# Optimization experiments

Measured on AMD Instinct MI355X. Metric: run time of the kernel, lower is better.

## Reference

```python
import jax, jax.numpy as jnp
import numpy as np


def setup_inputs() -> dict:
    key = jax.random.key(0)
    ks = jax.random.split(key, 7)
    C = 512
    x = jax.random.normal(ks[0], (16, C, 64, 64), dtype=jnp.float32)
    wq = jax.random.normal(ks[1], (C, C), dtype=jnp.float32) * (1.0 / np.sqrt(C))
    bq = jax.random.normal(ks[2], (C,), dtype=jnp.float32) * 0.02
    wk = jax.random.normal(ks[3], (C, C), dtype=jnp.float32) * (1.0 / np.sqrt(C))
    bk = jax.random.normal(ks[4], (C,), dtype=jnp.float32) * 0.02
    wo = jax.random.normal(ks[5], (C, C), dtype=jnp.float32) * (1.0 / np.sqrt(C))
    bo = jax.random.normal(ks[6], (C,), dtype=jnp.float32) * 0.02
    return {"x": x, "wq": wq, "bq": bq, "wk": wk, "bk": bk, "wo": wo, "bo": bo, "num_heads": 8}


def _conv1x1(x, w, b):
    # 1x1 conv == per-pixel linear map over channels; w: [Cout, Cin]
    return jnp.einsum('oc,bchw->bohw', w, x) + b[None, :, None, None]


def reference(x, wq, bq, wk, bk, wo, bo, num_heads):
    B, C, H, W = x.shape
    dh = C // num_heads
    P = H * W  # spatial positions (tokens)
    q = _conv1x1(x, wq, bq).reshape(B, num_heads, dh, P)
    k = _conv1x1(x, wk, bk).reshape(B, num_heads, dh, P)
    v = x.reshape(B, num_heads, dh, P)
    # NOTE: faithful to the torch code, attention is [B, nh, dh, dh]
    # (channel-channel scores contracted over spatial positions).
    att = jnp.einsum('bndp,bnep->bnde', q, k) / jnp.sqrt(jnp.asarray(dh, x.dtype))
    att = jax.nn.softmax(att, axis=-1)
    out = jnp.einsum('bnde,bnep->bndp', att, v).reshape(B, C, H, W)
    out = _conv1x1(out, wo, bo)
    return out + x
```

## Files before the change

kernel.cpp:

```cpp
#include <hip/hip_runtime.h>


typedef unsigned short ushort_t;
typedef __attribute__((ext_vector_type(8))) short bf16x8;
typedef __attribute__((ext_vector_type(4))) float f32x4;
typedef __attribute__((ext_vector_type(4))) unsigned short us4;
typedef __attribute__((ext_vector_type(8))) unsigned short us8;

#define NB 16
#define NC 512
#define NP 4096
#define NHD 8
#define DH 64

#define BM 128
#define BN 128
#define BKK 64

__device__ inline ushort_t f2bf(float f) {
  unsigned int u = __float_as_uint(f);
  u += 0x7FFFu + ((u >> 16) & 1u);
  return (ushort_t)(u >> 16);
}
__device__ inline float bf2f(ushort_t h) {
  return __uint_as_float(((unsigned int)h) << 16);
}

__device__ inline void gld_lds16(const void* g, void* l) {
  __builtin_amdgcn_global_load_lds(
      (const __attribute__((address_space(1))) unsigned int*)g,
      (__attribute__((address_space(3))) unsigned int*)l, 16, 0, 0);
}

__global__ __launch_bounds__(256, 4) void k_mfma_bt(
    const ushort_t* __restrict__ A, const ushort_t* __restrict__ B,
    void* __restrict__ Cv, const float* __restrict__ bias,
    int lda, int ldb, int ldc, long long sA, long long sB, long long sC,
    int Kper, int mode, int flags) {
  __shared__ __align__(128) ushort_t Smem[16640];
  ushort_t* As = Smem;
  ushort_t* Bs = Smem + 8320;
  int m0, n0;
  long long zc;
  const ushort_t *Ab, *Bb;
  if (flags & 2) {
    int flat = blockIdx.x + 10 * blockIdx.z;
    int nf = (flat & 7) * 80 + (flat >> 3);
    int z2 = nf / 10, tile = nf - z2 * 10;
    int bb = z2 >> 2, sp = z2 & 3;
    int tm = (0x1A449000u >> (tile * 3)) & 7;
    int tn = (0x1B4D1688u >> (tile * 3)) & 7;
    m0 = tm * BM; n0 = tn * BN;
    Ab = A + bb * sA + (long long)sp * Kper;
    Bb = B + bb * sB + (long long)sp * Kper;
    zc = (long long)z2 * sC;
  } else {
    int bx = blockIdx.x, by = blockIdx.y;
    if (flags & 1) {
      int nxy = gridDim.x * gridDim.y;
      int id = bx + gridDim.x * by;
      int nid = (id & 7) * (nxy >> 3) + (id >> 3);
      bx = nid % gridDim.x; by = nid / gridDim.x;
    }
    m0 = by * BM; n0 = bx * BN;
    Ab = A + blockIdx.z * sA;
    Bb = B + blockIdx.z * sB;
    zc = (long long)blockIdx.z * sC;
  }
  int t = threadIdx.x;
  int lane = t & 63, w = t >> 6;
  int wr = w >> 1, wc = w & 1;
  int l15 = lane & 15, l4 = lane >> 4;
  int sr = lane >> 3, scc = lane & 7;

  f32x4 zero = {0.f, 0.f, 0.f, 0.f};
  f32x4 acc[4][4];
#pragma unroll
  for (int i = 0; i < 4; ++i)
#pragma unroll
    for (int j = 0; j < 4; ++j) acc[i][j] = zero;

  for (int k0 = 0; k0 < Kper; k0 += BKK) {
#pragma unroll
    for (int i = 0; i < 4; ++i) {
      int slab = w * 4 + i;
      int r = slab * 8 + sr;
      int kc = scc ^ (r & 7);
      gld_lds16(Ab + (size_t)(m0 + r) * lda + k0 + kc * 8, &As[slab * 512]);
      gld_lds16(Bb + (size_t)(n0 + r) * ldb + k0 + kc * 8, &Bs[slab * 512]);
    }
    __syncthreads();
#pragma unroll
    for (int kf = 0; kf < 2; ++kf) {
      bf16x8 av[4], bv[4];
#pragma unroll
      for (int i = 0; i < 4; ++i) {
        int r = wr * 64 + i * 16 + l15;
        int c = (kf * 4 + l4) ^ (r & 7);
        av[i] = *(const bf16x8*)&As[r * 64 + c * 8];
        int rn = wc * 64 + i * 16 + l15;
        int cn = (kf * 4 + l4) ^ (rn & 7);
        bv[i] = *(const bf16x8*)&Bs[rn * 64 + cn * 8];
      }
#pragma unroll
      for (int i = 0; i < 4; ++i)
#pragma unroll
        for (int j = 0; j < 4; ++j)
          acc[i][j] = __builtin_amdgcn_mfma_f32_16x16x32_bf16(av[i], bv[j],
                                                              acc[i][j], 0, 0, 0);
    }
    __syncthreads();
  }

  if (mode == 3) {
    ushort_t* C = (ushort_t*)Cv + zc;
#pragma unroll
    for (int i = 0; i < 4; ++i)
#pragma unroll
      for (int j = 0; j < 4; ++j)
#pragma unroll
        for (int rr = 0; rr < 4; ++rr) {
          int grow = m0 + wr * 64 + i * 16 + l4 * 4 + rr;
          int gcol = n0 + wc * 64 + j * 16 + l15;
          float v = acc[i][j][rr];
          ushort_t hi = f2bf(v);
          C[(size_t)grow * ldc + gcol] = hi;
          C[4194304 + (size_t)grow * ldc + gcol] = f2bf(v - bf2f(hi));
        }
  } else {
    float* C = (float*)Cv + zc;
    float* fbuf = (float*)Smem;
#pragma unroll
    for (int ch = 0; ch < 2; ++ch) {
      if (wr == ch) {
#pragma unroll
        for (int i = 0; i < 4; ++i)
#pragma unroll
          for (int j = 0; j < 4; ++j)
#pragma unroll
            for (int rr = 0; rr < 4; ++rr)
              fbuf[(i * 16 + l4 * 4 + rr) * 130 + wc * 64 + j * 16 + l15] =
                  acc[i][j][rr];
      }
      __syncthreads();
      {
        int row = t >> 2, q = t & 3;
        int grow = m0 + ch * 64 + row;
        float bb = (mode == 1) ? bias[grow] : 0.f;
        float* crow = C + (size_t)grow * ldc + n0 + q * 32;
#pragma unroll
        for (int u = 0; u < 8; ++u) {
          f32x4 v = *reinterpret_cast<const f32x4*>(&fbuf[row * 130 + q * 32 + u * 4]);
          v[0] += bb; v[1] += bb; v[2] += bb; v[3] += bb;
          if (mode == 1)
            __builtin_nontemporal_store(v, reinterpret_cast<f32x4*>(crow + u * 4));
          else
            *reinterpret_cast<f32x4*>(crow + u * 4) = v;
        }
      }
      __syncthreads();
    }
  }
}

__global__ __launch_bounds__(256) void k_prep(const float* __restrict__ x,
                                              ushort_t* __restrict__ xbf,
                                              ushort_t* __restrict__ xt,
                                              float* __restrict__ sPart) {
  __shared__ ushort_t ldsC[128 * 132];
  int b = blockIdx.z;
  int pp0 = blockIdx.x * 128, cc0 = blockIdx.y * 128;
  const float* xb = x + ((size_t)b * NC + cc0) * NP + pp0;
  int t = threadIdx.x;
  int rq = t >> 5;
  int q  = t & 31;
#pragma unroll
  for (int i = 0; i < 16; ++i) {
    int r = i * 8 + rq;
    float4 v = *reinterpret_cast<const float4*>(xb + (size_t)r * NP + q * 4);
    us4 u = {f2bf(v.x), f2bf(v.y), f2bf(v.z), f2bf(v.w)};
    *reinterpret_cast<us4*>(&xbf[((size_t)b * NC + cc0 + r) * NP + pp0 + q * 4]) = u;
    *reinterpret_cast<us4*>(&ldsC[r * 132 + q * 4]) = u;
    float s4 = (v.x + v.y) + (v.z + v.w);
    s4 += __shfl_xor(s4, 1, 32);
    s4 += __shfl_xor(s4, 2, 32);
    s4 += __shfl_xor(s4, 4, 32);
    s4 += __shfl_xor(s4, 8, 32);
    s4 += __shfl_xor(s4, 16, 32);
    if (q == 0) sPart[(size_t)blockIdx.x * (NB * NC) + b * NC + cc0 + r] = s4;
  }
  __syncthreads();
  int p = t >> 1, chalf = (t & 1) * 64;
  ushort_t* dst = &xt[((size_t)b * NP + pp0 + p) * NC + cc0 + chalf];
#pragma unroll
  for (int g = 0; g < 8; ++g) {
    us8 o;
#pragma unroll
    for (int j = 0; j < 8; ++j) o[j] = ldsC[(chalf + g * 8 + j) * 132 + p];
    *reinterpret_cast<us8*>(dst + g * 8) = o;
  }
}

__global__ __launch_bounds__(256) void k_sreduce(const float* __restrict__ sPart,
                                                 float* __restrict__ s) {
  int idx = blockIdx.x * 256 + threadIdx.x;
  float a = 0.f;
  for (int pb = 0; pb < 32; ++pb) a += sPart[(size_t)pb * (NB * NC) + idx];
  s[idx] = a;
}

__global__ __launch_bounds__(256) void k_cvtw(
    const float* __restrict__ wq, const float* __restrict__ wk,
    const float* __restrict__ wo, ushort_t* __restrict__ q,
    ushort_t* __restrict__ k, ushort_t* __restrict__ o) {
  int i = blockIdx.x * 256 + threadIdx.x;
  q[i] = f2bf(wq[i]);
  k[i] = f2bf(wk[i]);
  o[i] = f2bf(wo[i]);
}

__global__ __launch_bounds__(256) void k_reduceG(const float* __restrict__ Gp,
                                                 ushort_t* __restrict__ Gb) {
  __shared__ ushort_t ldsM[128 * 36];
  int slab = blockIdx.x, tile = blockIdx.y, b = blockIdx.z;
  int tm = (0x1A449000u >> (tile * 3)) & 7;
  int tn = (0x1B4D1688u >> (tile * 3)) & 7;
  int t = threadIdx.x;
  const float* base = Gp + ((size_t)b * 4) * 262144 +
                      (size_t)(tm * 128) * 512 + tn * 128 + slab * 32;
  ushort_t* gb = Gb + (size_t)b * 262144;
#pragma unroll
  for (int i = 0; i < 4; ++i) {
    int idx = i * 256 + t;
    int r = idx >> 3, lq = idx & 7;
    const float* p = base + (size_t)r * 512 + lq * 4;
    float4 v0 = *reinterpret_cast<const float4*>(p);
    float4 v1 = *reinterpret_cast<const float4*>(p + 262144);
    float4 v2 = *reinterpret_cast<const float4*>(p + 2 * 262144);
    float4 v3 = *reinterpret_cast<const float4*>(p + 3 * 262144);
    us4 u = {f2bf((v0.x + v1.x) + (v2.x + v3.x)),
             f2bf((v0.y + v1.y) + (v2.y + v3.y)),
             f2bf((v0.z + v1.z) + (v2.z + v3.z)),
             f2bf((v0.w + v1.w) + (v2.w + v3.w))};
    *reinterpret_cast<us4*>(
        &gb[(size_t)(tm * 128 + r) * 512 + tn * 128 + slab * 32 + lq * 4]) = u;
    if (tm != tn) *reinterpret_cast<us4*>(&ldsM[r * 36 + lq * 4]) = u;
  }
  if (tm == tn) return;
  __syncthreads();
  int orow = t >> 3, og = t & 7;
  ushort_t* dst = &gb[(size_t)(tn * 128 + slab * 32 + orow) * 512 + tm * 128 + og * 16];
#pragma unroll
  for (int h = 0; h < 2; ++h) {
    us8 o;
#pragma unroll
    for (int j = 0; j < 8; ++j) o[j] = ldsM[(og * 16 + h * 8 + j) * 36 + orow];
    *reinterpret_cast<us8*>(dst + h * 8) = o;
  }
}

__global__ __launch_bounds__(256) void k_uw(
    const float* __restrict__ wq, const float* __restrict__ wk,
    const float* __restrict__ s, float* __restrict__ U, float* __restrict__ W) {
  int b = blockIdx.x >> 3, n = blockIdx.x & 7;
  int t = threadIdx.x;
  __shared__ float ssh[NC];
  for (int i = t; i < NC; i += 256) ssh[i] = s[b * NC + i];
  __syncthreads();
  int pair = t >> 1, half = t & 1;
  int d = pair & 63, sel = pair >> 6;
  const float* row = (sel ? wk : wq) + (size_t)(n * DH + d) * NC + half * 256;
  const float* sb = ssh + half * 256;
  float a = 0.f;
#pragma unroll 8
  for (int i = 0; i < 64; ++i) {
    float4 v = reinterpret_cast<const float4*>(row)[i];
    a += v.x * sb[i * 4] + v.y * sb[i * 4 + 1] + v.z * sb[i * 4 + 2] +
         v.w * sb[i * 4 + 3];
  }
  a += __shfl_xor(a, 1, 64);
  if (half == 0) (sel ? W : U)[b * NC + n * DH + d] = a;
}

__global__ __launch_bounds__(256) void k_fused(
    const ushort_t* __restrict__ Thi, const ushort_t* __restrict__ Tlo,
    const ushort_t* __restrict__ Wkb, const ushort_t* __restrict__ Wob,
    const float* __restrict__ U, const float* __restrict__ Wv,
    const float* __restrict__ bq, const float* __restrict__ bk,
    ushort_t* __restrict__ Mb) {
  __shared__ __align__(128) ushort_t Th[64 * 64];
  __shared__ __align__(128) ushort_t Tl[64 * 64];
  __shared__ __align__(128) ushort_t Wks[64 * 64];
  __shared__ float Ps[64][65];
  __shared__ __align__(16) ushort_t PT[64 * 72];
  __shared__ __align__(128) ushort_t Wos[128 * 64];
  __shared__ float ush[64], wsh[64], bqs[64], bks[64];

  int b = blockIdx.x >> 4, n = (blockIdx.x >> 1) & 7, half = blockIdx.x & 1;
  int t = threadIdx.x, lane = t & 63, w = t >> 6;
  int l15 = lane & 15, l4 = lane >> 4;

  if (t < 64) ush[t] = U[b * NC + n * DH + t];
  else if (t < 128) wsh[t - 64] = Wv[b * NC + n * DH + (t - 64)];
  else if (t < 192) bqs[t - 128] = bq[n * DH + (t - 128)];
  else bks[t - 192] = bk[n * DH + (t - 192)];

  const size_t tbase = ((size_t)b * NC + n * DH) * NC;
  f32x4 zero = {0.f, 0.f, 0.f, 0.f};
  f32x4 acc[4];
#pragma unroll
  for (int i = 0; i < 4; ++i) acc[i] = zero;

  for (int kc0 = 0; kc0 < NC; kc0 += 64) {
    __syncthreads();
#pragma unroll
    for (int i = 0; i < 6; ++i) {
      int slab = w * 6 + i;
      int mat = slab >> 3, sl = slab & 7;
      int r = sl * 8 + (lane >> 3);
      int kc = (lane & 7) ^ (r & 7);
      if (mat == 0)
        gld_lds16(Thi + tbase + (size_t)r * NC + kc0 + kc * 8, &Th[sl * 512]);
      else if (mat == 1)
        gld_lds16(Tlo + tbase + (size_t)r * NC + kc0 + kc * 8, &Tl[sl * 512]);
      else
        gld_lds16(Wkb + (size_t)(n * DH + r) * NC + kc0 + kc * 8, &Wks[sl * 512]);
    }
    __syncthreads();
#pragma unroll
    for (int kf = 0; kf < 2; ++kf) {
      int rn = w * 16 + l15;
      int cn = (kf * 4 + l4) ^ (rn & 7);
      bf16x8 bvf = *(const bf16x8*)&Wks[rn * 64 + cn * 8];
#pragma unroll
      for (int i = 0; i < 4; ++i) {
        int r = i * 16 + l15;
        int c = (kf * 4 + l4) ^ (r & 7);
        bf16x8 ah = *(const bf16x8*)&Th[r * 64 + c * 8];
        bf16x8 al = *(const bf16x8*)&Tl[r * 64 + c * 8];
        acc[i] = __builtin_amdgcn_mfma_f32_16x16x32_bf16(ah, bvf, acc[i], 0, 0, 0);
        acc[i] = __builtin_amdgcn_mfma_f32_16x16x32_bf16(al, bvf, acc[i], 0, 0, 0);
      }
    }
  }
#pragma unroll
  for (int i = 0; i < 4; ++i)
#pragma unroll
    for (int rr = 0; rr < 4; ++rr) {
      int d = i * 16 + l4 * 4 + rr, e = w * 16 + l15;
      float v = acc[i][rr] + ush[d] * bks[e] + bqs[d] * (wsh[e] + 4096.f * bks[e]);
      Ps[d][e] = v * 0.125f;
    }
  __syncthreads();
  {
    int d = w * 16 + l15;
    float mx = -1e30f;
#pragma unroll
    for (int i = 0; i < 16; ++i) mx = fmaxf(mx, Ps[d][l4 * 16 + i]);
    mx = fmaxf(mx, __shfl_xor(mx, 16, 64));
    mx = fmaxf(mx, __shfl_xor(mx, 32, 64));
    float pv[16];
    float sum = 0.f;
#pragma unroll
    for (int i = 0; i < 16; ++i) {
      pv[i] = __expf(Ps[d][l4 * 16 + i] - mx);
      sum += pv[i];
    }
    sum += __shfl_xor(sum, 16, 64);
    sum += __shfl_xor(sum, 32, 64);
    float inv = 1.f / sum;
#pragma unroll
    for (int i = 0; i < 16; ++i) PT[(l4 * 16 + i) * 72 + d] = f2bf(pv[i] * inv);
  }
  for (int mi = 0; mi < 2; ++mi) {
    int mt = half * 2 + mi;
    __syncthreads();
#pragma unroll
    for (int i = 0; i < 4; ++i) {
      int slab = w * 4 + i;
      int r = slab * 8 + (lane >> 3);
      int kc = (lane & 7) ^ (r & 7);
      gld_lds16(Wob + (size_t)(mt * 128 + r) * NC + n * DH + kc * 8,
                &Wos[slab * 512]);
    }
    __syncthreads();
    f32x4 acc2[2][4];
#pragma unroll
    for (int i2 = 0; i2 < 2; ++i2)
#pragma unroll
      for (int j = 0; j < 4; ++j) acc2[i2][j] = zero;
#pragma unroll
    for (int kf = 0; kf < 2; ++kf) {
      bf16x8 bv[4];
#pragma unroll
      for (int j = 0; j < 4; ++j) {
        int e = j * 16 + l15;
        bv[j] = *(const bf16x8*)&PT[e * 72 + (kf * 4 + l4) * 8];
      }
#pragma unroll
      for (int i2 = 0; i2 < 2; ++i2) {
        int r = w * 32 + i2 * 16 + l15;
        int c = (kf * 4 + l4) ^ (r & 7);
        bf16x8 av = *(const bf16x8*)&Wos[r * 64 + c * 8];
#pragma unroll
        for (int j = 0; j < 4; ++j)
          acc2[i2][j] =
              __builtin_amdgcn_mfma_f32_16x16x32_bf16(av, bv[j], acc2[i2][j], 0, 0, 0);
      }
    }
#pragma unroll
    for (int i2 = 0; i2 < 2; ++i2)
#pragma unroll
      for (int j = 0; j < 4; ++j)
#pragma unroll
        for (int rr = 0; rr < 4; ++rr) {
          int grow = mt * 128 + w * 32 + i2 * 16 + l4 * 4 + rr;
          int gcol = n * DH + j * 16 + l15;
          float v = acc2[i2][j][rr];
          if (grow == gcol) v += 1.f;
          Mb[((size_t)b * NC + grow) * NC + gcol] = f2bf(v);
        }
  }
}

#define BKt 32
#define BMt 128
#define BNt 128
#define LDTK 132

__global__ __launch_bounds__(256) void k_rowsum(const float* __restrict__ x,
                                                float* __restrict__ s) {
  int row = blockIdx.x;
  const float* xr = x + (size_t)row * NP;
  int t = threadIdx.x;
  float acc = 0.f;
  for (int i = t; i < NP / 4; i += 256) {
    float4 v = reinterpret_cast<const float4*>(xr)[i];
    acc += (v.x + v.y) + (v.z + v.w);
  }
  for (int off = 32; off > 0; off >>= 1) acc += __shfl_down(acc, off, 64);
  __shared__ float red[4];
  int lane = t & 63, wv = t >> 6;
  if (lane == 0) red[wv] = acc;
  __syncthreads();
  if (t == 0) s[row] = (red[0] + red[1]) + (red[2] + red[3]);
}

__global__ __launch_bounds__(256) void k_gemm_abT(
    const float* __restrict__ Abase, const float* __restrict__ Bbase,
    float* __restrict__ Cbase, int K, int lda, int ldb, int ldc,
    size_t sA, size_t sB, size_t sC) {
  __shared__ float As[BKt][LDTK];
  __shared__ float Bs[BKt][LDTK];
  const float* A = Abase + sA * blockIdx.z;
  const float* Bm = Bbase + sB * blockIdx.z;
  float* Cm = Cbase + sC * blockIdx.z;
  int m0 = blockIdx.y * BMt, n0 = blockIdx.x * BNt;
  int t = threadIdx.x;
  int tr = t >> 4, tc = t & 15;
  float acc[8][8];
#pragma unroll
  for (int i = 0; i < 8; ++i)
#pragma unroll
    for (int j = 0; j < 8; ++j) acc[i][j] = 0.f;
  for (int k0 = 0; k0 < K; k0 += BKt) {
#pragma unroll
    for (int it = 0; it < 4; ++it) {
      int idx = it * 256 + t;
      int r = idx >> 3, kq = idx & 7;
      float4 va = *reinterpret_cast<const float4*>(A + (size_t)(m0 + r) * lda + k0 + kq * 4);
      As[kq * 4 + 0][r] = va.x; As[kq * 4 + 1][r] = va.y;
      As[kq * 4 + 2][r] = va.z; As[kq * 4 + 3][r] = va.w;
      float4 vb = *reinterpret_cast<const float4*>(Bm + (size_t)(n0 + r) * ldb + k0 + kq * 4);
      Bs[kq * 4 + 0][r] = vb.x; Bs[kq * 4 + 1][r] = vb.y;
      Bs[kq * 4 + 2][r] = vb.z; Bs[kq * 4 + 3][r] = vb.w;
    }
    __syncthreads();
#pragma unroll
    for (int kk = 0; kk < BKt; ++kk) {
      float4 a0 = *reinterpret_cast<const float4*>(&As[kk][tr * 8]);
      float4 a1 = *reinterpret_cast<const float4*>(&As[kk][tr * 8 + 4]);
      float4 b0 = *reinterpret_cast<const float4*>(&Bs[kk][tc * 8]);
      float4 b1 = *reinterpret_cast<const float4*>(&Bs[kk][tc * 8 + 4]);
      float av[8] = {a0.x, a0.y, a0.z, a0.w, a1.x, a1.y, a1.z, a1.w};
      float bv[8] = {b0.x, b0.y, b0.z, b0.w, b1.x, b1.y, b1.z, b1.w};
#pragma unroll
      for (int i = 0; i < 8; ++i)
#pragma unroll
        for (int j = 0; j < 8; ++j) acc[i][j] += av[i] * bv[j];
    }
    __syncthreads();
  }
#pragma unroll
  for (int i = 0; i < 8; ++i) {
    float* crow = Cm + (size_t)(m0 + tr * 8 + i) * ldc + n0 + tc * 8;
    float4 c0 = {acc[i][0], acc[i][1], acc[i][2], acc[i][3]};
    float4 c1 = {acc[i][4], acc[i][5], acc[i][6], acc[i][7]};
    *reinterpret_cast<float4*>(crow) = c0;
    *reinterpret_cast<float4*>(crow + 4) = c1;
  }
}

__global__ __launch_bounds__(256) void k_gemm_ab(
    const float* __restrict__ Abase, const float* __restrict__ Bbase,
    float* __restrict__ Cbase, const float* __restrict__ bias,
    int K, int lda, int ldb, int ldc, size_t sA, size_t sB, size_t sC) {
  __shared__ float As[BKt][LDTK];
  __shared__ float Bs[BKt][LDTK];
  const float* A = Abase + sA * blockIdx.z;
  const float* Bm = Bbase + sB * blockIdx.z;
  float* Cm = Cbase + sC * blockIdx.z;
  int m0 = blockIdx.y * BMt, n0 = blockIdx.x * BNt;
  int t = threadIdx.x;
  int tr = t >> 4, tc = t & 15;
  float acc[8][8];
#pragma unroll
  for (int i = 0; i < 8; ++i)
#pragma unroll
    for (int j = 0; j < 8; ++j) acc[i][j] = 0.f;
  for (int k0 = 0; k0 < K; k0 += BKt) {
#pragma unroll
    for (int it = 0; it < 4; ++it) {
      int idx = it * 256 + t;
      int r = idx >> 3, kq = idx & 7;
      float4 va = *reinterpret_cast<const float4*>(A + (size_t)(m0 + r) * lda + k0 + kq * 4);
      As[kq * 4 + 0][r] = va.x; As[kq * 4 + 1][r] = va.y;
      As[kq * 4 + 2][r] = va.z; As[kq * 4 + 3][r] = va.w;
      int kk = idx >> 5, nq = idx & 31;
      float4 vb = *reinterpret_cast<const float4*>(Bm + (size_t)(k0 + kk) * ldb + n0 + nq * 4);
      *reinterpret_cast<float4*>(&Bs[kk][nq * 4]) = vb;
    }
    __syncthreads();
#pragma unroll
    for (int kk = 0; kk < BKt; ++kk) {
      float4 a0 = *reinterpret_cast<const float4*>(&As[kk][tr * 8]);
      float4 a1 = *reinterpret_cast<const float4*>(&As[kk][tr * 8 + 4]);
      float4 b0 = *reinterpret_cast<const float4*>(&Bs[kk][tc * 8]);
      float4 b1 = *reinterpret_cast<const float4*>(&Bs[kk][tc * 8 + 4]);
      float av[8] = {a0.x, a0.y, a0.z, a0.w, a1.x, a1.y, a1.z, a1.w};
      float bv[8] = {b0.x, b0.y, b0.z, b0.w, b1.x, b1.y, b1.z, b1.w};
#pragma unroll
      for (int i = 0; i < 8; ++i)
#pragma unroll
        for (int j = 0; j < 8; ++j) acc[i][j] += av[i] * bv[j];
    }
    __syncthreads();
  }
#pragma unroll
  for (int i = 0; i < 8; ++i) {
    int row = m0 + tr * 8 + i;
    float bb = bias ? bias[row] : 0.f;
    float* crow = Cm + (size_t)row * ldc + n0 + tc * 8;
    float4 c0 = {acc[i][0] + bb, acc[i][1] + bb, acc[i][2] + bb, acc[i][3] + bb};
    float4 c1 = {acc[i][4] + bb, acc[i][5] + bb, acc[i][6] + bb, acc[i][7] + bb};
    *reinterpret_cast<float4*>(crow) = c0;
    *reinterpret_cast<float4*>(crow + 4) = c1;
  }
}

__global__ __launch_bounds__(256) void k_att(
    const float* __restrict__ T, const float* __restrict__ wq,
    const float* __restrict__ bq, const float* __restrict__ wk,
    const float* __restrict__ bk, const float* __restrict__ wo,
    const float* __restrict__ s, float* __restrict__ Mf) {
  int b = blockIdx.x >> 3, n = blockIdx.x & 7;
  int t = threadIdx.x;
  __shared__ float sh_s[NC];
  __shared__ float sh_u[DH], sh_w[DH];
  __shared__ float L[DH][DH + 1];
  __shared__ float Ts[DH][68];
  __shared__ float Ks[DH][68];

  for (int i = t; i < NC; i += 256) sh_s[i] = s[b * NC + i];
  __syncthreads();
  if (t < 128) {
    int d = t & 63;
    const float* wrow = (t < 64 ? wq : wk) + (size_t)(n * DH + d) * NC;
    float a = 0.f;
    for (int c = 0; c < NC; ++c) a += wrow[c] * sh_s[c];
    if (t < 64) sh_u[d] = a; else sh_w[d] = a;
  }

  int d = t >> 2, eg = t & 3;
  float acc[16];
#pragma unroll
  for (int i = 0; i < 16; ++i) acc[i] = 0.f;

  for (int c0 = 0; c0 < NC; c0 += 64) {
#pragma unroll
    for (int it = 0; it < 4; ++it) {
      int idx = it * 256 + t;
      int r = idx >> 4, cq = idx & 15;
      float4 v = *reinterpret_cast<const float4*>(
          T + ((size_t)b * NC + n * DH + r) * NC + c0 + cq * 4);
      *reinterpret_cast<float4*>(&Ts[r][cq * 4]) = v;
      float4 kv = *reinterpret_cast<const float4*>(
          wk + (size_t)(n * DH + r) * NC + c0 + cq * 4);
      Ks[cq * 4 + 0][r] = kv.x; Ks[cq * 4 + 1][r] = kv.y;
      Ks[cq * 4 + 2][r] = kv.z; Ks[cq * 4 + 3][r] = kv.w;
    }
    __syncthreads();
    for (int cc = 0; cc < 64; ++cc) {
      float tv = Ts[d][cc];
      float4 k0v = *reinterpret_cast<const float4*>(&Ks[cc][eg * 16]);
      float4 k1v = *reinterpret_cast<const float4*>(&Ks[cc][eg * 16 + 4]);
      float4 k2v = *reinterpret_cast<const float4*>(&Ks[cc][eg * 16 + 8]);
      float4 k3v = *reinterpret_cast<const float4*>(&Ks[cc][eg * 16 + 12]);
      acc[0] += tv * k0v.x;  acc[1] += tv * k0v.y;
      acc[2] += tv * k0v.z;  acc[3] += tv * k0v.w;
      acc[4] += tv * k1v.x;  acc[5] += tv * k1v.y;
      acc[6] += tv * k1v.z;  acc[7] += tv * k1v.w;
      acc[8] += tv * k2v.x;  acc[9] += tv * k2v.y;
      acc[10] += tv * k2v.z; acc[11] += tv * k2v.w;
      acc[12] += tv * k3v.x; acc[13] += tv * k3v.y;
      acc[14] += tv * k3v.z; acc[15] += tv * k3v.w;
    }
    __syncthreads();
  }

  float bqd = bq[n * DH + d];
  float ud = sh_u[d];
#pragma unroll
  for (int i = 0; i < 16; ++i) {
    int e = eg * 16 + i;
    float bke = bk[n * DH + e];
    L[d][e] = (acc[i] + ud * bke + bqd * (sh_w[e] + (float)NP * bke)) * 0.125f;
  }
  __syncthreads();
  if (t < 64) {
    float mx = -1e30f;
    for (int e = 0; e < DH; ++e) mx = fmaxf(mx, L[t][e]);
    float sum = 0.f;
    for (int e = 0; e < DH; ++e) { float p = __expf(L[t][e] - mx); L[t][e] = p; sum += p; }
    float inv = 1.f / sum;
    for (int e = 0; e < DH; ++e) L[t][e] *= inv;
  }
  __syncthreads();

#pragma unroll
  for (int rep = 0; rep < 2; ++rep) {
    int o = rep * 256 + t;
    const float* worow = wo + (size_t)o * NC + n * DH;
    float wreg[64];
#pragma unroll
    for (int q = 0; q < 16; ++q) {
      float4 v = *reinterpret_cast<const float4*>(worow + q * 4);
      wreg[q * 4 + 0] = v.x; wreg[q * 4 + 1] = v.y;
      wreg[q * 4 + 2] = v.z; wreg[q * 4 + 3] = v.w;
    }
    for (int e = 0; e < DH; ++e) {
      float a = 0.f;
#pragma unroll
      for (int dd = 0; dd < DH; ++dd) a += wreg[dd] * L[dd][e];
      int col = n * DH + e;
      if (o == col) a += 1.f;
      Mf[((size_t)b * NC + o) * NC + col] = a;
    }
  }
}

extern "C" void kernel_launch(void* const* d_in, const int* in_sizes, int n_in,
                              void* d_out, int out_size, void* d_ws, size_t ws_size,
                              hipStream_t stream) {
  const float* x  = (const float*)d_in[0];
  const float* wq = (const float*)d_in[1];
  const float* bq = (const float*)d_in[2];
  const float* wk = (const float*)d_in[3];
  const float* bk = (const float*)d_in[4];
  const float* wo = (const float*)d_in[5];
  const float* bo = (const float*)d_in[6];
  float* out = (float*)d_out;
  char* ws = (char*)d_ws;

  const size_t sX = (size_t)NC * NP;
  const size_t sG = (size_t)NC * NC;
  const size_t xbf_bytes = (size_t)NB * sX * 2;

  size_t off_s  = 0;
  size_t off_sp = 32768;
  size_t off_xt = off_sp + (size_t)64 * NB * NC * 4;
  size_t off_mb = off_xt + xbf_bytes;
  size_t off_wq = off_mb + (size_t)NB * sG * 2;
  size_t off_wk = off_wq + sG * 2;
  size_t off_wo = off_wk + sG * 2;
  size_t off_u  = off_wo + sG * 2;
  size_t off_w  = off_u + 32768;
  size_t need   = off_w + 32768;

  if (ws_size >= need + 4096) {
    float*    s     = (float*)(ws + off_s);
    float*    sPart = (float*)(ws + off_sp);
    ushort_t* Xt    = (ushort_t*)(ws + off_xt);
    ushort_t* Mb    = (ushort_t*)(ws + off_mb);
    ushort_t* Wqb   = (ushort_t*)(ws + off_wq);
    ushort_t* Wkb   = (ushort_t*)(ws + off_wk);
    ushort_t* Wob   = (ushort_t*)(ws + off_wo);
    float*    U     = (float*)(ws + off_u);
    float*    W     = (float*)(ws + off_w);
    char* dob = (char*)d_out;
    ushort_t* Xbf   = (ushort_t*)d_out;
    float*    Gpart = (float*)(dob + xbf_bytes);
    ushort_t* Gb    = (ushort_t*)d_out;
    ushort_t* Thi   = (ushort_t*)(dob + xbf_bytes);
    ushort_t* Tlo   = Thi + 4194304;

    k_cvtw<<<dim3(1024), 256, 0, stream>>>(wq, wk, wo, Wqb, Wkb, Wob);
    k_prep<<<dim3(32, 4, 16), 256, 0, stream>>>(x, Xbf, Xt, sPart);
    k_sreduce<<<dim3(32), 256, 0, stream>>>(sPart, s);
    k_uw<<<dim3(NB * NHD), 256, 0, stream>>>(wq, wk, s, U, W);
    k_mfma_bt<<<dim3(10, 1, 64), 256, 0, stream>>>(
        Xbf, Xbf, Gpart, nullptr, NP, NP, NC,
        (long long)sX, (long long)sX, (long long)sG, NP / 4, 2, 2);
    k_reduceG<<<dim3(4, 10, 16), 256, 0, stream>>>(Gpart, Gb);
    k_mfma_bt<<<dim3(4, 4, 16), 256, 0, stream>>>(
        Wqb, Gb, Thi, nullptr, NC, NC, NC,
        0LL, (long long)sG, (long long)sG, NC, 3, 1);
    k_fused<<<dim3(NB * NHD * 2), 256, 0, stream>>>(Thi, Tlo, Wkb, Wob, U, W,
                                                    bq, bk, Mb);
    k_mfma_bt<<<dim3(32, 4, 16), 256, 0, stream>>>(
        Mb, Xt, out, bo, NC, NC, NP,
        (long long)sG, (long long)sX, (long long)sX, NC, 1, 1);
  } else {
    float* s  = (float*)ws;
    float* G  = (float*)(ws + 32768);
    float* Tm = (float*)(ws + 32768 + (size_t)NB * sG * 4);
    float* M  = G;
    k_rowsum<<<NB * NC, 256, 0, stream>>>(x, s);
    k_gemm_abT<<<dim3(4, 4, NB), 256, 0, stream>>>(x, x, G, NP, NP, NP, NC, sX, sX, sG);
    k_gemm_ab<<<dim3(4, 4, NB), 256, 0, stream>>>(wq, G, Tm, nullptr, NC, NC, NC, NC,
                                                  0, sG, sG);
    k_att<<<NB * NHD, 256, 0, stream>>>(Tm, wq, bq, wk, bk, wo, s, M);
    k_gemm_ab<<<dim3(NP / BNt, NC / BMt, NB), 256, 0, stream>>>(M, x, out, bo, NC, NC,
                                                                NP, NP, sG, sX, sX);
  }
}
```

Measured before the change: 236.1 us.

## Split prep into row-wise convert+rowsum and separate bf16 transpose kernel

Replaces the fused convert/transpose/partial-sum prep kernel and its partial-sum reduction with two kernels. One converts each x row to bf16 and computes the full row sum directly. The other re-reads the bf16 tensor and transposes it through a larger LDS tile with nontemporal stores. This removes the partial-sum buffer and the extra reduction launch, but adds a second pass over the bf16 data (about 64MB read) in exchange for simpler, more coalesced access patterns.

```diff
diff --git a/kernel.cpp b/kernel.cpp
--- a/kernel.cpp
+++ b/kernel.cpp
@@ -163,50 +163,53 @@
   }
 }
 
-__global__ __launch_bounds__(256) void k_prep(const float* __restrict__ x,
-                                              ushort_t* __restrict__ xbf,
-                                              ushort_t* __restrict__ xt,
-                                              float* __restrict__ sPart) {
-  __shared__ ushort_t ldsC[128 * 132];
+__global__ __launch_bounds__(256) void k_cvt_rowsum(const float* __restrict__ x,
+                                                    ushort_t* __restrict__ xbf,
+                                                    float* __restrict__ s) {
+  int row = blockIdx.x;
+  const float* xr = x + (size_t)row * NP;
+  ushort_t* xo = xbf + (size_t)row * NP;
+  int t = threadIdx.x;
+  float acc = 0.f;
+#pragma unroll
+  for (int i = 0; i < 4; ++i) {
+    int idx = i * 256 + t;
+    float4 v = reinterpret_cast<const float4*>(xr)[idx];
+    us4 u = {f2bf(v.x), f2bf(v.y), f2bf(v.z), f2bf(v.w)};
+    reinterpret_cast<us4*>(xo)[idx] = u;
+    acc += (v.x + v.y) + (v.z + v.w);
+  }
+  for (int off = 32; off > 0; off >>= 1) acc += __shfl_down(acc, off, 64);
+  __shared__ float red[4];
+  if ((t & 63) == 0) red[t >> 6] = acc;
+  __syncthreads();
+  if (t == 0) s[row] = (red[0] + red[1]) + (red[2] + red[3]);
+}
+
+__global__ __launch_bounds__(256, 2) void k_transp(const ushort_t* __restrict__ xbf,
+                                                   ushort_t* __restrict__ xt) {
+  __shared__ ushort_t lds[256 * 128];
   int b = blockIdx.z;
-  int pp0 = blockIdx.x * 128, cc0 = blockIdx.y * 128;
-  const float* xb = x + ((size_t)b * NC + cc0) * NP + pp0;
-  int t = threadIdx.x;
-  int rq = t >> 5;
-  int q  = t & 31;
+  int pp0 = blockIdx.x * 128, cc0 = blockIdx.y * 256;
+  int t = threadIdx.x;
+  int cr = t >> 4, ck = t & 15;
 #pragma unroll
   for (int i = 0; i < 16; ++i) {
-    int r = i * 8 + rq;
-    float4 v = *reinterpret_cast<const float4*>(xb + (size_t)r * NP + q * 4);
-    us4 u = {f2bf(v.x), f2bf(v.y), f2bf(v.z), f2bf(v.w)};
-    *reinterpret_cast<us4*>(&xbf[((size_t)b * NC + cc0 + r) * NP + pp0 + q * 4]) = u;
-    *reinterpret_cast<us4*>(&ldsC[r * 132 + q * 4]) = u;
-    float s4 = (v.x + v.y) + (v.z + v.w);
-    s4 += __shfl_xor(s4, 1, 32);
-    s4 += __shfl_xor(s4, 2, 32);
-    s4 += __shfl_xor(s4, 4, 32);
-    s4 += __shfl_xor(s4, 8, 32);
-    s4 += __shfl_xor(s4, 16, 32);
-    if (q == 0) sPart[(size_t)blockIdx.x * (NB * NC) + b * NC + cc0 + r] = s4;
-  }
-  __syncthreads();
-  int p = t >> 1, chalf = (t & 1) * 64;
-  ushort_t* dst = &xt[((size_t)b * NP + pp0 + p) * NC + cc0 + chalf];
-#pragma unroll
-  for (int g = 0; g < 8; ++g) {
+    int c = i * 16 + cr;
+    us8 v = *reinterpret_cast<const us8*>(
+        &xbf[((size_t)b * NC + cc0 + c) * NP + pp0 + ck * 8]);
+    *reinterpret_cast<us8*>(&lds[c * 128 + ck * 8]) = v;
+  }
+  __syncthreads();
+  int p = t >> 1, h = t & 1;
+  ushort_t* dst = &xt[((size_t)b * NP + pp0 + p) * NC + cc0 + h * 128];
+#pragma unroll
+  for (int g = 0; g < 16; ++g) {
     us8 o;
 #pragma unroll
-    for (int j = 0; j < 8; ++j) o[j] = ldsC[(chalf + g * 8 + j) * 132 + p];
-    *reinterpret_cast<us8*>(dst + g * 8) = o;
-  }
-}
-
-__global__ __launch_bounds__(256) void k_sreduce(const float* __restrict__ sPart,
-                                                 float* __restrict__ s) {
-  int idx = blockIdx.x * 256 + threadIdx.x;
-  float a = 0.f;
-  for (int pb = 0; pb < 32; ++pb) a += sPart[(size_t)pb * (NB * NC) + idx];
-  s[idx] = a;
+    for (int j = 0; j < 8; ++j) o[j] = lds[(h * 128 + g * 8 + j) * 128 + p];
+    __builtin_nontemporal_store(o, reinterpret_cast<us8*>(dst + g * 8));
+  }
 }
 
 __global__ __launch_bounds__(256) void k_cvtw(
@@ -689,7 +692,6 @@
 
   if (ws_size >= need + 4096) {
     float*    s     = (float*)(ws + off_s);
-    float*    sPart = (float*)(ws + off_sp);
     ushort_t* Xt    = (ushort_t*)(ws + off_xt);
     ushort_t* Mb    = (ushort_t*)(ws + off_mb);
     ushort_t* Wqb   = (ushort_t*)(ws + off_wq);
@@ -705,8 +707,8 @@
     ushort_t* Tlo   = Thi + 4194304;
 
     k_cvtw<<<dim3(1024), 256, 0, stream>>>(wq, wk, wo, Wqb, Wkb, Wob);
-    k_prep<<<dim3(32, 4, 16), 256, 0, stream>>>(x, Xbf, Xt, sPart);
-    k_sreduce<<<dim3(32), 256, 0, stream>>>(sPart, s);
+    k_cvt_rowsum<<<dim3(NB * NC), 256, 0, stream>>>(x, Xbf, s);
+    k_transp<<<dim3(32, 2, 16), 256, 0, stream>>>(Xbf, Xt);
     k_uw<<<dim3(NB * NHD), 256, 0, stream>>>(wq, wk, s, U, W);
     k_mfma_bt<<<dim3(10, 1, 64), 256, 0, stream>>>(
         Xbf, Xbf, Gpart, nullptr, NP, NP, NC,
```

Result: slower. 356.5 us (+51.0%).
